# Optimization experiments

Hardware: AMD Instinct MI355X
Metric: run time of the kernel (lower is better)

The kernel has to match this reference:

```python
import jax, jax.numpy as jnp
import numpy as np

C_IN = 12      # total channels (rgb-noised + hidden)
C_NOISE = 3    # noise-prediction channels
HID = 128      # rule-MLP hidden size
PERC = 48      # perception channels (depthwise, 48/12 = 4 filters per channel)
TDIM = 256     # sinusoidal time-embedding dim


def setup_inputs() -> dict:
    key = jax.random.key(0)
    ks = jax.random.split(key, 12)
    B, H, W = 16, 256, 256
    x = jax.random.normal(ks[0], (B, C_NOISE, H, W), jnp.float32)
    hidden_channels = jax.random.normal(ks[1], (B, C_IN - C_NOISE, H, W), jnp.float32)
    t = jax.random.randint(ks[2], (B,), 0, 1000)
    # depthwise 3x3 perceive conv: torch weight shape [out=48, in/groups=1, 3, 3]
    w_perceive = jax.random.normal(ks[3], (PERC, 1, 3, 3), jnp.float32) * 0.1
    b_perceive = jax.random.normal(ks[4], (PERC,), jnp.float32) * 0.01
    # 1x1 convs of the rule network, stored as [out, in]
    w1 = jax.random.normal(ks[5], (HID, PERC), jnp.float32) * 0.1
    b1 = jax.random.normal(ks[6], (HID,), jnp.float32) * 0.01
    w2 = jax.random.normal(ks[7], (HID, HID), jnp.float32) * 0.05
    b2 = jax.random.normal(ks[8], (HID,), jnp.float32) * 0.01
    # conv3 is zero-initialized in the original; random here for test coverage
    w3 = jax.random.normal(ks[9], (C_IN, HID), jnp.float32) * 0.05
    # time embedding Linear(256 -> c_noise)
    w_time = jax.random.normal(ks[10], (C_NOISE, TDIM), jnp.float32) * 0.1
    b_time = jax.random.normal(ks[11], (C_NOISE,), jnp.float32) * 0.01
    return dict(x=x, hidden_channels=hidden_channels, t=t,
                w_perceive=w_perceive, b_perceive=b_perceive,
                w1=w1, b1=b1, w2=w2, b2=b2, w3=w3,
                w_time=w_time, b_time=b_time)


def _pos_encoding(t, channels):
    # t: [B] int -> [B, channels] sinusoidal embedding (torch repeat-then-scale layout)
    inv_freq = 1.0 / (10000.0 ** (jnp.arange(0, channels, 2, dtype=jnp.float32) / channels))
    ang = t.astype(jnp.float32)[:, None] * inv_freq  # [B, channels//2]
    return jnp.concatenate([jnp.sin(ang), jnp.cos(ang)], axis=-1)


def reference(x, hidden_channels, t, w_perceive, b_perceive, w1, b1, w2, b2, w3, w_time, b_time):
    # concat noised channels with hidden state channels -> [B, 12, H, W]
    xf = jnp.concatenate([x, hidden_channels], axis=1)
    # depthwise 3x3 conv, 'same' padding, groups = C_IN
    perc = jax.lax.conv_general_dilated(
        xf, w_perceive, window_strides=(1, 1), padding='SAME',
        feature_group_count=C_IN,
        dimension_numbers=('NCHW', 'OIHW', 'NCHW')) + b_perceive[None, :, None, None]
    # rule network: three 1x1 convs (pointwise MLP) with ReLUs
    h = jax.nn.relu(jnp.einsum('bchw,oc->bohw', perc, w1) + b1[None, :, None, None])
    h = jax.nn.relu(jnp.einsum('bchw,oc->bohw', h, w2) + b2[None, :, None, None])
    out = jnp.einsum('bchw,oc->bohw', h, w3)  # no bias
    # time embedding: sinusoidal -> SiLU -> Linear -> broadcast over H, W
    pe = _pos_encoding(t, TDIM)                       # [B, 256]
    emb = jax.nn.silu(pe) @ w_time.T + b_time         # [B, 3]
    noise_prediction = out[:, :C_NOISE] + emb[:, :, None, None]
    hidden_out = out[:, C_NOISE:]
    return (hidden_out, noise_prediction)
```

## Files before the change

kernel.cpp:

```cpp
#include <hip/hip_runtime.h>


#define ACT_S 136
#define NOISE_BASE 9437184

#define WSF_OFF 13312
#define WSF_BP 0
#define WSF_B1 48
#define WSF_B2 176
#define WSF_WP 304
#define WSF_EMB 736

typedef short bf16x8 __attribute__((ext_vector_type(8)));
typedef float f32x4 __attribute__((ext_vector_type(4)));

__device__ __forceinline__ short f2bf(float f) {
    union { float f; unsigned u; } cv; cv.f = f;
    unsigned r = cv.u + 0x7FFFu + ((cv.u >> 16) & 1u);
    return (short)(r >> 16);
}
__device__ __forceinline__ unsigned pk2bf(float f0, float f1) {
    union { float f; unsigned u; } a, b; a.f = f0; b.f = f1;
    return __builtin_amdgcn_perm(b.u + 0x8000u, a.u + 0x8000u, 0x07060302u);
}

__global__ void prep_emb_kernel(const float* __restrict__ wpg, const float* __restrict__ bpg,
                                const float* __restrict__ w1g, const float* __restrict__ b1g,
                                const float* __restrict__ w2g, const float* __restrict__ b2g,
                                const float* __restrict__ w3g,
                                const int* __restrict__ t,
                                const float* __restrict__ wt, const float* __restrict__ bt,
                                short* __restrict__ wsb, float* __restrict__ wsf)
{
    if (blockIdx.x < 107) {
        int i = blockIdx.x * 256 + threadIdx.x;
        if (i < 8192) {
            int o = i >> 6, c = i & 63;
            wsb[i] = (c < 48) ? f2bf(w1g[o * 48 + c]) : (short)0;
        } else if (i < 24576) {
            wsb[i] = f2bf(w2g[i - 8192]);
        } else if (i < 26624) {
            int k = i - 24576;
            wsb[i] = (k < 1536) ? f2bf(w3g[k]) : (short)0;
        } else if (i < 26672) {
            wsf[WSF_BP + (i - 26624)] = bpg[i - 26624];
        } else if (i < 26800) {
            wsf[WSF_B1 + (i - 26672)] = b1g[i - 26672];
        } else if (i < 26928) {
            wsf[WSF_B2 + (i - 26800)] = b2g[i - 26800];
        } else if (i < 27360) {
            int idx = i - 26928;
            int oc = idx / 9, k = idx % 9;
            wsf[WSF_WP + k * 48 + oc] = wpg[idx];
        }
        return;
    }
    int b = blockIdx.x - 107;
    int lane = threadIdx.x;
    if (lane >= 64) return;
    float tv = (float)t[b];
    float s0 = 0.f, s1 = 0.f, s2 = 0.f;
    const float LOG1E4 = 9.210340371976184f;
    #pragma unroll
    for (int ii = 0; ii < 2; ++ii) {
        int i = lane + ii * 64;
        float invf = __expf(-LOG1E4 * (float)i * (1.0f / 128.0f));
        float ang = tv * invf;
        float sn = sinf(ang), cs = cosf(ang);
        float ss = sn / (1.0f + __expf(-sn));
        float sc = cs / (1.0f + __expf(-cs));
        s0 += ss * wt[0 * 256 + i] + sc * wt[0 * 256 + i + 128];
        s1 += ss * wt[1 * 256 + i] + sc * wt[1 * 256 + i + 128];
        s2 += ss * wt[2 * 256 + i] + sc * wt[2 * 256 + i + 128];
    }
    #pragma unroll
    for (int off = 32; off; off >>= 1) {
        s0 += __shfl_down(s0, off);
        s1 += __shfl_down(s1, off);
        s2 += __shfl_down(s2, off);
    }
    if (lane == 0) {
        wsf[WSF_EMB + b * 3 + 0] = s0 + bt[0];
        wsf[WSF_EMB + b * 3 + 1] = s1 + bt[1];
        wsf[WSF_EMB + b * 3 + 2] = s2 + bt[2];
    }
}

__global__ __launch_bounds__(256, 4) void canet_main(
    const float* __restrict__ xg,
    const float* __restrict__ hg,
    const short* __restrict__ wsb,
    const float* __restrict__ wsf,
    float* __restrict__ outg)
{
    __shared__ __align__(16) short bufA[64 * ACT_S];
    __shared__ __align__(16) short h1S[64 * ACT_S];
    __shared__ __align__(16) short w3_s[12 * 128];
    __shared__ __align__(16) float wpT_s[9 * 48];
    __shared__ __align__(16) float bias_s[256];
    __shared__ __align__(16) float bp_s[48];

    const int tid = threadIdx.x;
    const int b = blockIdx.x >> 8;
    const int y = blockIdx.x & 255;

    for (int i = tid; i < 432; i += 256) wpT_s[i] = wsf[WSF_WP + i];
    if (tid < 48) bp_s[tid] = wsf[WSF_BP + tid];
    bias_s[tid] = wsf[WSF_B1 + tid];
    for (int i = tid; i < 1536; i += 256) {
        int row = i >> 7, col = i & 127;
        w3_s[(row << 7) + (col ^ ((row & 7) << 3))] = wsb[24576 + i];
    }

    const int wv = tid >> 6;
    const int lane = tid & 63;
    const int m = lane & 15;
    const int q = lane >> 4;

    bf16x8 w1f[2][2], w2f[2][4];
    #pragma unroll
    for (int j = 0; j < 2; ++j) {
        int n = wv * 32 + j * 16 + m;
        #pragma unroll
        for (int ks = 0; ks < 2; ++ks)
            w1f[j][ks] = *(const bf16x8*)(wsb + n * 64 + ks * 32 + q * 8);
        #pragma unroll
        for (int ks = 0; ks < 4; ++ks)
            w2f[j][ks] = *(const bf16x8*)(wsb + 8192 + n * 128 + ks * 32 + q * 8);
    }
    const float embv = (m < 3) ? wsf[WSF_EMB + b * 3 + m] : 0.0f;

    const float* src3[3];
    #pragma unroll
    for (int i3 = 0; i3 < 3; ++i3) {
        int ic = 3 * q + i3;
        src3[i3] = (ic < 3) ? (xg + (((size_t)b * 3 + ic) << 16))
                            : (hg + (((size_t)b * 9 + (ic - 3)) << 16));
    }

    const int mm = (m < 12) ? m : 11;
    const int w3sw = (mm & 7) << 3;

    __syncthreads();

    for (int it = 0; it < 4; ++it) {
        const int x0 = it * 64;
        const int px = x0 + wv * 16 + m;

        {
            const int xm1 = px - (px > 0);
            const int xp1 = px + (px < 255);
            const bool okl = (px > 0), okr = (px < 255);
            short* prow = bufA + (wv * 16 + m) * ACT_S;
            const bool interior = (y >= 1) && (y <= 254);
            #pragma unroll
            for (int i3 = 0; i3 < 3; ++i3) {
                const float* s = src3[i3];
                float tap[9];
                if (interior) {
                    #pragma unroll
                    for (int ky = 0; ky < 3; ++ky) {
                        const float* rp = s + (y + ky - 1) * 256;
                        float c0 = rp[xm1], c1 = rp[px], c2 = rp[xp1];
                        tap[ky * 3 + 0] = okl ? c0 : 0.0f;
                        tap[ky * 3 + 1] = c1;
                        tap[ky * 3 + 2] = okr ? c2 : 0.0f;
                    }
                } else {
                    #pragma unroll
                    for (int ky = 0; ky < 3; ++ky) {
                        int yy = y + ky - 1;
                        bool yok = (yy >= 0) && (yy < 256);
                        const float* rp = s + (yok ? yy : y) * 256;
                        float c0 = rp[xm1], c1 = rp[px], c2 = rp[xp1];
                        tap[ky * 3 + 0] = (yok && okl) ? c0 : 0.0f;
                        tap[ky * 3 + 1] = yok ? c1 : 0.0f;
                        tap[ky * 3 + 2] = (yok && okr) ? c2 : 0.0f;
                    }
                }
                f32x4 a4 = *(const f32x4*)(bp_s + 12 * q + 4 * i3);
                #pragma unroll
                for (int k = 0; k < 9; ++k) {
                    f32x4 w4 = *(const f32x4*)(wpT_s + k * 48 + 12 * q + 4 * i3);
                    float t = tap[k];
                    a4[0] += w4[0] * t; a4[1] += w4[1] * t;
                    a4[2] += w4[2] * t; a4[3] += w4[3] * t;
                }
                uint2 pk;
                pk.x = pk2bf(a4[0], a4[1]);
                pk.y = pk2bf(a4[2], a4[3]);
                *(uint2*)(prow + 12 * q + 4 * i3) = pk;
            }
            *(uint2*)(prow + 48 + 4 * q) = uint2{0u, 0u};
        }
        __syncthreads();

        #pragma unroll
        for (int nt = 0; nt < 4; ++nt) {
            f32x4 c0 = *(const f32x4*)(bias_s + wv * 32 + q * 4);
            f32x4 c1 = *(const f32x4*)(bias_s + wv * 32 + 16 + q * 4);
            #pragma unroll
            for (int ks = 0; ks < 2; ++ks) {
                bf16x8 p = *(const bf16x8*)(bufA + (nt * 16 + m) * ACT_S + ks * 32 + q * 8);
                c0 = __builtin_amdgcn_mfma_f32_16x16x32_bf16(w1f[0][ks], p, c0, 0, 0, 0);
                c1 = __builtin_amdgcn_mfma_f32_16x16x32_bf16(w1f[1][ks], p, c1, 0, 0, 0);
            }
            short* drow = h1S + (nt * 16 + m) * ACT_S + wv * 32 + q * 4;
            uint2 pk;
            pk.x = pk2bf(fmaxf(c0[0], 0.f), fmaxf(c0[1], 0.f));
            pk.y = pk2bf(fmaxf(c0[2], 0.f), fmaxf(c0[3], 0.f));
            *(uint2*)drow = pk;
            pk.x = pk2bf(fmaxf(c1[0], 0.f), fmaxf(c1[1], 0.f));
            pk.y = pk2bf(fmaxf(c1[2], 0.f), fmaxf(c1[3], 0.f));
            *(uint2*)(drow + 16) = pk;
        }
        __syncthreads();

        #pragma unroll
        for (int nt = 0; nt < 4; ++nt) {
            f32x4 c0 = *(const f32x4*)(bias_s + 128 + wv * 32 + q * 4);
            f32x4 c1 = *(const f32x4*)(bias_s + 128 + wv * 32 + 16 + q * 4);
            #pragma unroll
            for (int ks = 0; ks < 4; ++ks) {
                bf16x8 a = *(const bf16x8*)(h1S + (nt * 16 + m) * ACT_S + ks * 32 + q * 8);
                c0 = __builtin_amdgcn_mfma_f32_16x16x32_bf16(w2f[0][ks], a, c0, 0, 0, 0);
                c1 = __builtin_amdgcn_mfma_f32_16x16x32_bf16(w2f[1][ks], a, c1, 0, 0, 0);
            }
            short* drow = bufA + (nt * 16 + m) * ACT_S + wv * 32 + q * 4;
            uint2 pk;
            pk.x = pk2bf(fmaxf(c0[0], 0.f), fmaxf(c0[1], 0.f));
            pk.y = pk2bf(fmaxf(c0[2], 0.f), fmaxf(c0[3], 0.f));
            *(uint2*)drow = pk;
            pk.x = pk2bf(fmaxf(c1[0], 0.f), fmaxf(c1[1], 0.f));
            pk.y = pk2bf(fmaxf(c1[2], 0.f), fmaxf(c1[3], 0.f));
            *(uint2*)(drow + 16) = pk;
        }
        __syncthreads();

        {
            f32x4 acc = {0.f, 0.f, 0.f, 0.f};
            #pragma unroll
            for (int ks = 0; ks < 4; ++ks) {
                bf16x8 a = *(const bf16x8*)(bufA + (wv * 16 + m) * ACT_S + ks * 32 + q * 8);
                bf16x8 w3k = *(const bf16x8*)(w3_s + (mm << 7) + ((ks * 32 + q * 8) ^ w3sw));
                acc = __builtin_amdgcn_mfma_f32_16x16x32_bf16(a, w3k, acc, 0, 0, 0);
            }
            if (m < 12) {
                int xx0 = x0 + wv * 16 + q * 4;
                size_t idx;
                if (m < 3) {
                    idx = (size_t)NOISE_BASE + (((size_t)b * 3 + m) << 16) + (size_t)y * 256 + xx0;
                } else {
                    idx = (((size_t)b * 9 + (m - 3)) << 16) + (size_t)y * 256 + xx0;
                }
                f32x4 vst = {acc[0] + embv, acc[1] + embv, acc[2] + embv, acc[3] + embv};
                *(f32x4*)(outg + idx) = vst;
            }
        }
        __syncthreads();
    }
}

extern "C" void kernel_launch(void* const* d_in, const int* in_sizes, int n_in,
                              void* d_out, int out_size, void* d_ws, size_t ws_size,
                              hipStream_t stream) {
    const float* xg  = (const float*)d_in[0];
    const float* hg  = (const float*)d_in[1];
    const int*   tg  = (const int*)  d_in[2];
    const float* wpg = (const float*)d_in[3];
    const float* bpg = (const float*)d_in[4];
    const float* w1g = (const float*)d_in[5];
    const float* b1g = (const float*)d_in[6];
    const float* w2g = (const float*)d_in[7];
    const float* b2g = (const float*)d_in[8];
    const float* w3g = (const float*)d_in[9];
    const float* wtg = (const float*)d_in[10];
    const float* btg = (const float*)d_in[11];
    float* outg = (float*)d_out;
    short* wsb  = (short*)d_ws;
    float* wsf  = (float*)d_ws + WSF_OFF;

    prep_emb_kernel<<<123, 256, 0, stream>>>(wpg, bpg, w1g, b1g, w2g, b2g, w3g,
                                             tg, wtg, btg, wsb, wsf);
    canet_main<<<4096, 256, 0, stream>>>(xg, hg, wsb, wsf, outg);
}
```

Baseline: 228.0 us.

## Fold depthwise perceive conv into first pointwise layer weights, feed raw taps to MFMA

New measurement: 246.7 us. 1.08x slower.

```diff
diff --git a/kernel.cpp b/kernel.cpp
--- a/kernel.cpp
+++ b/kernel.cpp
@@ -4,12 +4,10 @@
 #define ACT_S 136
 #define NOISE_BASE 9437184
 
-#define WSF_OFF 13312
-#define WSF_BP 0
-#define WSF_B1 48
-#define WSF_B2 176
-#define WSF_WP 304
-#define WSF_EMB 736
+#define WSF_OFF 17408
+#define WSF_B1 0
+#define WSF_B2 128
+#define WSF_EMB 256
 
 typedef short bf16x8 __attribute__((ext_vector_type(8)));
 typedef float f32x4 __attribute__((ext_vector_type(4)));
@@ -32,30 +30,44 @@
                                 const float* __restrict__ wt, const float* __restrict__ bt,
                                 short* __restrict__ wsb, float* __restrict__ wsf)
 {
-    if (blockIdx.x < 107) {
-        int i = blockIdx.x * 256 + threadIdx.x;
-        if (i < 8192) {
-            int o = i >> 6, c = i & 63;
-            wsb[i] = (c < 48) ? f2bf(w1g[o * 48 + c]) : (short)0;
-        } else if (i < 24576) {
-            wsb[i] = f2bf(w2g[i - 8192]);
-        } else if (i < 26624) {
-            int k = i - 24576;
-            wsb[i] = (k < 1536) ? f2bf(w3g[k]) : (short)0;
-        } else if (i < 26672) {
-            wsf[WSF_BP + (i - 26624)] = bpg[i - 26624];
-        } else if (i < 26800) {
-            wsf[WSF_B1 + (i - 26672)] = b1g[i - 26672];
-        } else if (i < 26928) {
-            wsf[WSF_B2 + (i - 26800)] = b2g[i - 26800];
-        } else if (i < 27360) {
-            int idx = i - 26928;
-            int oc = idx / 9, k = idx % 9;
-            wsf[WSF_WP + k * 48 + oc] = wpg[idx];
-        }
-        return;
-    }
-    int b = blockIdx.x - 107;
+    const int bid = blockIdx.x, tid = threadIdx.x;
+    if (bid < 64) {
+        int i = bid * 256 + tid;
+        int o = i >> 7, kk = i & 127;
+        int qq = kk >> 5, r = kk & 31;
+        float v = 0.f;
+        if (r < 30 && (r % 10) < 9) {
+            int c3 = r / 10, k = r % 10;
+            int ic = 3 * qq + c3;
+            #pragma unroll
+            for (int j = 0; j < 4; ++j)
+                v += w1g[o * 48 + 4 * ic + j] * wpg[(4 * ic + j) * 9 + k];
+        }
+        wsb[i] = f2bf(v);
+        return;
+    }
+    if (bid < 128) {
+        int i = (bid - 64) * 256 + tid;
+        wsb[16384 + i] = f2bf(w2g[i]);
+        return;
+    }
+    if (bid == 128) {
+        for (int j = tid; j < 2048; j += 256)
+            wsb[32768 + j] = (j < 1536) ? f2bf(w3g[j]) : (short)0;
+        return;
+    }
+    if (bid == 129) {
+        if (tid < 128) {
+            float s = b1g[tid];
+            #pragma unroll 4
+            for (int c = 0; c < 48; ++c) s += w1g[tid * 48 + c] * bpg[c];
+            wsf[WSF_B1 + tid] = s;
+        } else {
+            wsf[WSF_B2 + (tid - 128)] = b2g[tid - 128];
+        }
+        return;
+    }
+    int b = bid - 130;
     int lane = threadIdx.x;
     if (lane >= 64) return;
     float tv = (float)t[b];
@@ -96,20 +108,16 @@
     __shared__ __align__(16) short bufA[64 * ACT_S];
     __shared__ __align__(16) short h1S[64 * ACT_S];
     __shared__ __align__(16) short w3_s[12 * 128];
-    __shared__ __align__(16) float wpT_s[9 * 48];
     __shared__ __align__(16) float bias_s[256];
-    __shared__ __align__(16) float bp_s[48];
 
     const int tid = threadIdx.x;
     const int b = blockIdx.x >> 8;
     const int y = blockIdx.x & 255;
 
-    for (int i = tid; i < 432; i += 256) wpT_s[i] = wsf[WSF_WP + i];
-    if (tid < 48) bp_s[tid] = wsf[WSF_BP + tid];
     bias_s[tid] = wsf[WSF_B1 + tid];
     for (int i = tid; i < 1536; i += 256) {
         int row = i >> 7, col = i & 127;
-        w3_s[(row << 7) + (col ^ ((row & 7) << 3))] = wsb[24576 + i];
+        w3_s[(row << 7) + (col ^ ((row & 7) << 3))] = wsb[32768 + i];
     }
 
     const int wv = tid >> 6;
@@ -117,16 +125,15 @@
     const int m = lane & 15;
     const int q = lane >> 4;
 
-    bf16x8 w1f[2][2], w2f[2][4];
+    bf16x8 w1f[2][4], w2f[2][4];
     #pragma unroll
     for (int j = 0; j < 2; ++j) {
         int n = wv * 32 + j * 16 + m;
         #pragma unroll
-        for (int ks = 0; ks < 2; ++ks)
-            w1f[j][ks] = *(const bf16x8*)(wsb + n * 64 + ks * 32 + q * 8);
-        #pragma unroll
-        for (int ks = 0; ks < 4; ++ks)
-            w2f[j][ks] = *(const bf16x8*)(wsb + 8192 + n * 128 + ks * 32 + q * 8);
+        for (int ks = 0; ks < 4; ++ks) {
+            w1f[j][ks] = *(const bf16x8*)(wsb + n * 128 + ks * 32 + q * 8);
+            w2f[j][ks] = *(const bf16x8*)(wsb + 16384 + n * 128 + ks * 32 + q * 8);
+        }
     }
     const float embv = (m < 3) ? wsf[WSF_EMB + b * 3 + m] : 0.0f;
 
@@ -151,7 +158,7 @@
             const int xm1 = px - (px > 0);
             const int xp1 = px + (px < 255);
             const bool okl = (px > 0), okr = (px < 255);
-            short* prow = bufA + (wv * 16 + m) * ACT_S;
+            short* prow = bufA + (wv * 16 + m) * ACT_S + 32 * q;
             const bool interior = (y >= 1) && (y <= 254);
             #pragma unroll
             for (int i3 = 0; i3 < 3; ++i3) {
@@ -178,20 +185,14 @@
                         tap[ky * 3 + 2] = (yok && okr) ? c2 : 0.0f;
                     }
                 }
-                f32x4 a4 = *(const f32x4*)(bp_s + 12 * q + 4 * i3);
-                #pragma unroll
-                for (int k = 0; k < 9; ++k) {
-                    f32x4 w4 = *(const f32x4*)(wpT_s + k * 48 + 12 * q + 4 * i3);
-                    float t = tap[k];
-                    a4[0] += w4[0] * t; a4[1] += w4[1] * t;
-                    a4[2] += w4[2] * t; a4[3] += w4[3] * t;
-                }
-                uint2 pk;
-                pk.x = pk2bf(a4[0], a4[1]);
-                pk.y = pk2bf(a4[2], a4[3]);
-                *(uint2*)(prow + 12 * q + 4 * i3) = pk;
-            }
-            *(uint2*)(prow + 48 + 4 * q) = uint2{0u, 0u};
+                unsigned* pw = (unsigned*)(prow + 10 * i3);
+                pw[0] = pk2bf(tap[0], tap[1]);
+                pw[1] = pk2bf(tap[2], tap[3]);
+                pw[2] = pk2bf(tap[4], tap[5]);
+                pw[3] = pk2bf(tap[6], tap[7]);
+                pw[4] = pk2bf(tap[8], 0.0f);
+            }
+            *(unsigned*)(prow + 30) = 0u;
         }
         __syncthreads();
 
@@ -200,7 +201,7 @@
             f32x4 c0 = *(const f32x4*)(bias_s + wv * 32 + q * 4);
             f32x4 c1 = *(const f32x4*)(bias_s + wv * 32 + 16 + q * 4);
             #pragma unroll
-            for (int ks = 0; ks < 2; ++ks) {
+            for (int ks = 0; ks < 4; ++ks) {
                 bf16x8 p = *(const bf16x8*)(bufA + (nt * 16 + m) * ACT_S + ks * 32 + q * 8);
                 c0 = __builtin_amdgcn_mfma_f32_16x16x32_bf16(w1f[0][ks], p, c0, 0, 0, 0);
                 c1 = __builtin_amdgcn_mfma_f32_16x16x32_bf16(w1f[1][ks], p, c1, 0, 0, 0);
@@ -280,7 +281,7 @@
     short* wsb  = (short*)d_ws;
     float* wsf  = (float*)d_ws + WSF_OFF;
 
-    prep_emb_kernel<<<123, 256, 0, stream>>>(wpg, bpg, w1g, b1g, w2g, b2g, w3g,
+    prep_emb_kernel<<<146, 256, 0, stream>>>(wpg, bpg, w1g, b1g, w2g, b2g, w3g,
                                              tg, wtg, btg, wsb, wsf);
     canet_main<<<4096, 256, 0, stream>>>(xg, hg, wsb, wsf, outg);
 }
```
